# Performance work log

Hardware: AMD Instinct MI355X
Metric: run time of the kernel (lower is better)

The kernel has to match this reference:

```python
import jax, jax.numpy as jnp
from jax import lax
import numpy as np

# dims
V, D, T = 30000, 300, 24          # vocab, glove dim, seq len
H = 256                            # tweet_out_size == z_dim
NT, NU = 6000, 4000                # tweet nodes, user nodes
N = NT + NU
F, Z = 512, 256                    # user_feat_size, z_dim
E = 80000
B = 2000                           # batch_size (source tweets)
H1, H2, HEADS = 64, 100, 8
NEG = 0.2                          # GATConv default negative_slope


def setup_inputs() -> dict:
    k = jax.random.split(jax.random.key(0), 32)
    r = lambda i, shape, s=0.05: (s * jax.random.normal(k[i], shape)).astype(jnp.float32)
    return {
        "user_text": jax.random.randint(k[0], (B, T), 0, V),
        "user_feats": jax.random.normal(k[1], (NU, F), jnp.float32),
        "graph_node_features": jax.random.randint(k[2], (NT, T), 0, V),
        "graph_edge_index": jax.random.randint(k[3], (2, E), 0, N),
        "tweet_emb": r(4, (V, D), 0.1),
        "w_ih0": r(5, (3 * H, D)), "w_hh0": r(6, (3 * H, H)),
        "b_ih0": r(7, (3 * H,)), "b_hh0": r(8, (3 * H,)),
        "w_ih1": r(9, (3 * H, H)), "w_hh1": r(10, (3 * H, H)),
        "b_ih1": r(11, (3 * H,)), "b_hh1": r(12, (3 * H,)),
        "h0": r(13, (2, NT, H), 1.0),
        "w_mu": r(14, (Z, F)), "b_mu": r(15, (Z,)),
        "w_lv": r(16, (Z, F)), "b_lv": r(17, (Z,)),
        "w_dec": r(18, (F, Z)), "b_dec": r(19, (F,)),
        "vae_eps": r(20, (NU, Z), 1.0),
        "w1": r(21, (H, HEADS * H1)), "a_src1": r(22, (HEADS, H1)),
        "a_dst1": r(23, (HEADS, H1)), "b1": r(24, (HEADS * H1,)),
        "w2": r(25, (HEADS * H1, H2)), "a_src2": r(26, (1, H2)),
        "a_dst2": r(27, (1, H2)), "b2": r(28, (H2,)),
    }


def _gru_layer(x_seq, h0, w_ih, w_hh, b_ih, b_hh):
    # x_seq: [T, B, in]; torch nn.GRU gate math
    def step(h, x):
        gi = x @ w_ih.T + b_ih
        gh = h @ w_hh.T + b_hh
        i_r, i_z, i_n = jnp.split(gi, 3, axis=-1)
        h_r, h_z, h_n = jnp.split(gh, 3, axis=-1)
        r = jax.nn.sigmoid(i_r + h_r)
        z = jax.nn.sigmoid(i_z + h_z)
        n = jnp.tanh(i_n + r * h_n)
        hn = (1.0 - z) * n + z * h
        return hn, hn
    h_last, out = lax.scan(step, h0, x_seq)
    return out, h_last


def _gat(x, src, dst, w, a_src, a_dst, bias, heads, out_ch, concat):
    # PyG GATConv (eval mode, self-loops already appended)
    n = x.shape[0]
    xp = (x @ w).reshape(n, heads, out_ch)          # [N, H, C]
    as_n = (xp * a_src).sum(-1)                     # [N, H]
    ad_n = (xp * a_dst).sum(-1)
    e = jax.nn.leaky_relu(as_n[src] + ad_n[dst], NEG)          # [E, H]
    emax = jax.ops.segment_max(e, dst, num_segments=n)         # edge-softmax over dst
    ee = jnp.exp(e - emax[dst])
    denom = jax.ops.segment_sum(ee, dst, num_segments=n)
    alpha = ee / denom[dst]
    out = jax.ops.segment_sum(xp[src] * alpha[:, :, None], dst, num_segments=n)
    out = out.reshape(n, heads * out_ch) if concat else out.mean(axis=1)
    return out + bias


def reference(user_text, user_feats, graph_node_features, graph_edge_index,
              tweet_emb, w_ih0, w_hh0, b_ih0, b_hh0, w_ih1, w_hh1, b_ih1, b_hh1,
              h0, w_mu, b_mu, w_lv, b_lv, w_dec, b_dec, vae_eps,
              w1, a_src1, a_dst1, b1, w2, a_src2, a_dst2, b2):
    # --- VAE user embedding ---
    mu = user_feats @ w_mu.T + b_mu
    logvar = user_feats @ w_lv.T + b_lv
    z = mu + jnp.exp(0.5 * logvar) * vae_eps        # reparameterized latent
    rec = z @ w_dec.T + b_dec
    kl_loss = (-0.5 * (1.0 + logvar - mu**2 - jnp.exp(logvar)).sum(-1)).mean()
    rec_loss = ((rec - user_feats) ** 2).mean()
    # --- tweet encoder: embedding lookup + 2-layer GRU ---
    xe = tweet_emb[graph_node_features].transpose(1, 0, 2)     # [T, NT, D]
    out0, _ = _gru_layer(xe, h0[0], w_ih0, w_hh0, b_ih0, b_hh0)
    _, hn = _gru_layer(out0, h0[1], w_ih1, w_hh1, b_ih1, b_hh1)  # [NT, H]
    # --- assemble node features: source tweets, users, other tweets ---
    x_in = jnp.concatenate([hn[:B], z, hn[B:]], axis=0)        # [N, H]
    loops = jnp.arange(x_in.shape[0])
    src = jnp.concatenate([graph_edge_index[0], loops])
    dst = jnp.concatenate([graph_edge_index[1], loops])
    x1 = _gat(x_in, src, dst, w1, a_src1, a_dst1, b1, HEADS, H1, True)
    x2 = _gat(x1, src, dst, w2, a_src2, a_dst2, b2, 1, H2, False)
    return x2, kl_loss, rec_loss
```

## Files before the change

### kernel.cpp

```cpp
#include <hip/hip_runtime.h>

#define V_ 30000
#define D_ 300
#define DP_ 320
#define T_ 24
#define H_ 256
#define NT_ 6000
#define NU_ 4000
#define N_ 10000
#define F_ 512
#define Z_ 256
#define E_ 80000
#define B_ 2000
#define H1_ 64
#define H2_ 100
#define HEADS_ 8
#define E2_ (E_ + N_)

typedef __bf16 bf16_t;
typedef bf16_t bf16x8 __attribute__((ext_vector_type(8)));
typedef float  f32x4  __attribute__((ext_vector_type(4)));

__device__ __forceinline__ void gll16(const bf16_t* g, bf16_t* l)
{
    __builtin_amdgcn_global_load_lds(
        (const __attribute__((address_space(1))) void*)g,
        (__attribute__((address_space(3))) void*)l, 16, 0, 0);
}

struct GCfg {
    const bf16_t* A; const bf16_t* B; const float* bias;
    float* Cf; bf16_t* Cb; int M, N, K, ldc;
    const int* gtok; int t0;
};

template<bool OUTBF>
__global__ __launch_bounds__(256) void mfma_gemm(GCfg g0, GCfg g1)
{
    const GCfg g = blockIdx.z ? g1 : g0;
    __shared__ __align__(16) bf16_t SMEM[16384];
    const int tid  = (int)threadIdx.x;
    const int wave = tid >> 6, lane = tid & 63;
    const int quad = lane >> 4, l16 = lane & 15;
    const int mq = (wave & 1) * 64, nq = (wave >> 1) * 64;

    int bx = (int)blockIdx.x, by = (int)blockIdx.y;
    {
        int gx = (int)gridDim.x, total = gx * (int)gridDim.y;
        if ((total & 7) == 0) {
            int L = by * gx + bx;
            int F = (L & 7) * (total >> 3) + (L >> 3);
            bx = F % gx;
            by = F / gx;
        }
    }
    const int mbase = by * 128, nbase = bx * 128;
    const int M = g.M, N = g.N, K = g.K, ldc = g.ldc;

    const bf16_t* agp[2];
    const bf16_t* bgp[2];
#pragma unroll
    for (int j = 0; j < 2; j++) {
        int i = wave * 128 + j * 64 + lane;
        int c = i >> 7, row = i & 127;
        int r = mbase + row; if (r >= M) r = M - 1;
        int src = g.gtok ? g.gtok[(r % NT_) * T_ + g.t0 + (r / NT_)] : r;
        agp[j] = g.A + (size_t)src * K + c * 8;
        int rb = nbase + row; if (rb >= N) rb = N - 1;
        bgp[j] = g.B + (size_t)rb * K + c * 8;
    }

    f32x4 acc[4][4];
#pragma unroll
    for (int mi = 0; mi < 4; mi++)
#pragma unroll
        for (int ni = 0; ni < 4; ni++) acc[mi][ni] = (f32x4){0.f, 0.f, 0.f, 0.f};

    auto stage = [&](int b, int k0) {
        bf16_t* ab = SMEM + b * 4096 + wave * 1024;
        bf16_t* bb = SMEM + 8192 + b * 4096 + wave * 1024;
        gll16(agp[0] + k0, ab);
        gll16(agp[1] + k0, ab + 512);
        gll16(bgp[0] + k0, bb);
        gll16(bgp[1] + k0, bb + 512);
    };

    const int niter = K >> 5;
    stage(0, 0);
    for (int ks = 0; ks < niter; ks++) {
        __syncthreads();
        if (ks + 1 < niter) stage((ks + 1) & 1, (ks + 1) * 32);
        const bf16_t* Ab = SMEM + (ks & 1) * 4096;
        const bf16_t* Bb = SMEM + 8192 + (ks & 1) * 4096;
        bf16x8 afr[4], bfr[4];
#pragma unroll
        for (int mi = 0; mi < 4; mi++)
            afr[mi] = *(const bf16x8*)(Ab + (size_t)(quad * 128 + mq + mi * 16 + l16) * 8);
#pragma unroll
        for (int ni = 0; ni < 4; ni++)
            bfr[ni] = *(const bf16x8*)(Bb + (size_t)(quad * 128 + nq + ni * 16 + l16) * 8);
#pragma unroll
        for (int mi = 0; mi < 4; mi++)
#pragma unroll
            for (int ni = 0; ni < 4; ni++)
                acc[mi][ni] = __builtin_amdgcn_mfma_f32_16x16x32_bf16(
                    afr[mi], bfr[ni], acc[mi][ni], 0, 0, 0);
    }

    if (OUTBF) {
        __syncthreads();
#pragma unroll
        for (int ni = 0; ni < 4; ni++) {
            int colc = nq + ni * 16 + l16;
            float bv = g.bias ? g.bias[nbase + colc] : 0.f;
            int cc = colc >> 3, off = colc & 7;
#pragma unroll
            for (int mi = 0; mi < 4; mi++)
#pragma unroll
                for (int r = 0; r < 4; r++) {
                    int row = mq + mi * 16 + quad * 4 + r;
                    int sw = (row ^ (row >> 3)) & 7;
                    SMEM[row * 128 + ((cc ^ sw) << 3) + off] =
                        (bf16_t)(acc[mi][ni][r] + bv);
                }
        }
        __syncthreads();
        {
            int row = tid >> 1, seg = tid & 1;
            int sw = (row ^ (row >> 3)) & 7;
            int growr = mbase + row;
            if (growr < M) {
#pragma unroll
                for (int q = 0; q < 8; q++) {
                    int cc = seg * 8 + q;
                    bf16x8 v = *(const bf16x8*)(SMEM + row * 128 + ((cc ^ sw) << 3));
                    *(bf16x8*)(g.Cb + (size_t)growr * ldc + nbase + cc * 8) = v;
                }
            }
        }
    } else {
#pragma unroll
        for (int ni = 0; ni < 4; ni++) {
            int col = nbase + nq + ni * 16 + l16;
            if (col >= N) continue;
            float bv = g.bias ? g.bias[col] : 0.f;
#pragma unroll
            for (int mi = 0; mi < 4; mi++)
#pragma unroll
                for (int r = 0; r < 4; r++) {
                    int row = mbase + mq + mi * 16 + quad * 4 + r;
                    if (row >= M) continue;
                    g.Cf[(size_t)row * ldc + col] = acc[mi][ni][r] + bv;
                }
        }
    }
}

struct MegaLay {
    const bf16_t* vocGi;
    const int*    gnf;
    const bf16_t* whh0;
    const bf16_t* wih1;
    const bf16_t* whh1;
    const float *bhh0, *bih1, *bhh1;
    const bf16_t* h0in;
    const bf16_t* h1in;
    bf16_t*       h1out;
};

__device__ __forceinline__ float rcp_(float x)
{
    float r;
    asm("v_rcp_f32 %0, %1" : "=v"(r) : "v"(x));
    return r;
}
__device__ __forceinline__ float sigm_(float x)
{
    return rcp_(1.f + __expf(-x));
}
__device__ __forceinline__ float tanh_(float x)
{
    x = fminf(fmaxf(x, -15.f), 15.f);
    float t = __expf(2.f * x);
    return 1.f - 2.f * rcp_(t + 1.f);
}

#define HSW(Hb, row, byte) ((char*)(Hb) + ((((row) * 512) + (byte)) ^ (((row) & 7) << 4)))

__global__ __launch_bounds__(512, 1) void gru_mega(MegaLay L)
{
    __shared__ __align__(16) bf16_t H0L[8192];
    __shared__ __align__(16) bf16_t H1L[8192];
    __shared__ int TOK[768];
    const int tid  = (int)threadIdx.x;
    const int wv   = tid >> 6, lane = tid & 63;
    const int quad = lane >> 4, l16 = lane & 15;
    const int row0 = (int)blockIdx.x * 32;

    for (int i = tid; i < 768; i += 512) {
        int gi = row0 * T_ + i; if (gi >= NT_ * T_) gi = NT_ * T_ - 1;
        TOK[i] = L.gnf[gi];
    }
#pragma unroll
    for (int i = 0; i < 2; i++) {
        int idx  = i * 512 + tid;
        int rowl = idx >> 5, seg = idx & 31;
        int grow = row0 + rowl; if (grow >= NT_) grow = NT_ - 1;
        *(bf16x8*)HSW(H0L, rowl, seg * 16) =
            *(const bf16x8*)(L.h0in + (size_t)grow * H_ + seg * 8);
        *(bf16x8*)HSW(H1L, rowl, seg * 16) =
            *(const bf16x8*)(L.h1in + (size_t)grow * H_ + seg * 8);
    }

    float bh0[3][2], brz1[2][2], bni1[2], bnh1[2];
#pragma unroll
    for (int jj = 0; jj < 2; jj++) {
        int col = wv * 32 + jj * 16 + l16;
        bh0[0][jj] = L.bhh0[col];
        bh0[1][jj] = L.bhh0[256 + col];
        bh0[2][jj] = L.bhh0[512 + col];
        brz1[0][jj] = L.bih1[col] + L.bhh1[col];
        brz1[1][jj] = L.bih1[256 + col] + L.bhh1[256 + col];
        bni1[jj]    = L.bih1[512 + col];
        bnh1[jj]    = L.bhh1[512 + col];
    }

    auto run_gemm = [&](auto&& loadA, const bf16_t* W,
                        f32x4 (&arz)[2][2][2], f32x4 (&an)[2][2]) {
#pragma unroll 2
        for (int ks = 0; ks < 8; ks++) {
            bf16x8 bfr[3][2];
#pragma unroll
            for (int g = 0; g < 3; g++)
#pragma unroll
                for (int jj = 0; jj < 2; jj++)
                    bfr[g][jj] = *(const bf16x8*)(W +
                        (((size_t)(g * 16 + wv * 2 + jj) * 8 + ks) << 9) + lane * 8);
            bf16x8 afr[2];
            loadA(afr, ks);
#pragma unroll
            for (int m = 0; m < 2; m++)
#pragma unroll
                for (int jj = 0; jj < 2; jj++) {
                    arz[m][0][jj] = __builtin_amdgcn_mfma_f32_16x16x32_bf16(
                        afr[m], bfr[0][jj], arz[m][0][jj], 0, 0, 0);
                    arz[m][1][jj] = __builtin_amdgcn_mfma_f32_16x16x32_bf16(
                        afr[m], bfr[1][jj], arz[m][1][jj], 0, 0, 0);
                    an[m][jj] = __builtin_amdgcn_mfma_f32_16x16x32_bf16(
                        afr[m], bfr[2][jj], an[m][jj], 0, 0, 0);
                }
        }
    };

    __syncthreads();

    for (int t = 0; t < T_; t++) {
        float gi[2][2][4][3];
#pragma unroll
        for (int m = 0; m < 2; m++)
#pragma unroll
            for (int r2 = 0; r2 < 4; r2++) {
                int rowl = m * 16 + quad * 4 + r2;
                const bf16_t* gp = L.vocGi +
                    (size_t)TOK[rowl * T_ + t] * (3 * H_);
#pragma unroll
                for (int jj = 0; jj < 2; jj++) {
                    int col = wv * 32 + jj * 16 + l16;
#pragma unroll
                    for (int g = 0; g < 3; g++)
                        gi[m][jj][r2][g] = (float)gp[g * 256 + col];
                }
            }

        f32x4 arz[2][2][2], an_i[2][2], an_h[2][2];
#pragma unroll
        for (int m = 0; m < 2; m++)
#pragma unroll
            for (int jj = 0; jj < 2; jj++) {
                arz[m][0][jj] = (f32x4){0.f, 0.f, 0.f, 0.f};
                arz[m][1][jj] = (f32x4){0.f, 0.f, 0.f, 0.f};
                an_h[m][jj]   = (f32x4){0.f, 0.f, 0.f, 0.f};
            }

        run_gemm([&](bf16x8* afr, int ks) {
#pragma unroll
            for (int m = 0; m < 2; m++)
                afr[m] = *(const bf16x8*)HSW(H0L, m * 16 + l16,
                                             ks * 64 + quad * 16);
        }, L.whh0, arz, an_h);
        __syncthreads();

#pragma unroll
        for (int m = 0; m < 2; m++)
#pragma unroll
            for (int jj = 0; jj < 2; jj++) {
                int col = wv * 32 + jj * 16 + l16;
#pragma unroll
                for (int r = 0; r < 4; r++) {
                    int rowl = m * 16 + quad * 4 + r;
                    float hold = (float)*(const bf16_t*)HSW(H0L, rowl, col * 2);
                    float rg = sigm_(gi[m][jj][r][0] + arz[m][0][jj][r] + bh0[0][jj]);
                    float zg = sigm_(gi[m][jj][r][1] + arz[m][1][jj][r] + bh0[1][jj]);
                    float ng = tanh_(gi[m][jj][r][2] +
                                     rg * (an_h[m][jj][r] + bh0[2][jj]));
                    *(bf16_t*)HSW(H0L, rowl, col * 2) =
                        (bf16_t)((1.f - zg) * ng + zg * hold);
                }
            }
        __syncthreads();

#pragma unroll
        for (int m = 0; m < 2; m++)
#pragma unroll
            for (int jj = 0; jj < 2; jj++) {
                arz[m][0][jj] = (f32x4){0.f, 0.f, 0.f, 0.f};
                arz[m][1][jj] = (f32x4){0.f, 0.f, 0.f, 0.f};
                an_i[m][jj]   = (f32x4){0.f, 0.f, 0.f, 0.f};
                an_h[m][jj]   = (f32x4){0.f, 0.f, 0.f, 0.f};
            }
        run_gemm([&](bf16x8* afr, int ks) {
#pragma unroll
            for (int m = 0; m < 2; m++)
                afr[m] = *(const bf16x8*)HSW(H0L, m * 16 + l16,
                                             ks * 64 + quad * 16);
        }, L.wih1, arz, an_i);
        run_gemm([&](bf16x8* afr, int ks) {
#pragma unroll
            for (int m = 0; m < 2; m++)
                afr[m] = *(const bf16x8*)HSW(H1L, m * 16 + l16,
                                             ks * 64 + quad * 16);
        }, L.whh1, arz, an_h);
        __syncthreads();

#pragma unroll
        for (int m = 0; m < 2; m++)
#pragma unroll
            for (int jj = 0; jj < 2; jj++) {
                int col = wv * 32 + jj * 16 + l16;
#pragma unroll
                for (int r = 0; r < 4; r++) {
                    int rowl = m * 16 + quad * 4 + r;
                    float hold = (float)*(const bf16_t*)HSW(H1L, rowl, col * 2);
                    float rg = sigm_(arz[m][0][jj][r] + brz1[0][jj]);
                    float zg = sigm_(arz[m][1][jj][r] + brz1[1][jj]);
                    float ng = tanh_(an_i[m][jj][r] + bni1[jj] +
                                     rg * (an_h[m][jj][r] + bnh1[jj]));
                    *(bf16_t*)HSW(H1L, rowl, col * 2) =
                        (bf16_t)((1.f - zg) * ng + zg * hold);
                }
            }
    }

    __syncthreads();
#pragma unroll
    for (int i = 0; i < 2; i++) {
        int idx  = i * 512 + tid;
        int rowl = idx >> 5, seg = idx & 31;
        int grow = row0 + rowl;
        if (grow < NT_) {
            bf16x8 v = *(const bf16x8*)HSW(H1L, rowl, seg * 16);
            *(bf16x8*)(L.h1out + (size_t)grow * H_ + seg * 8) = v;
        }
    }
}

struct SegD { const float* src; bf16_t* dst; int rows, cin, cout, transp; };
struct PrepArgs { SegD seg[11]; long long base[12]; int nseg; long long total; };

__global__ void prep_kern(PrepArgs pa)
{
    long long stride = (long long)gridDim.x * blockDim.x;
    for (long long i = (long long)blockIdx.x * blockDim.x + threadIdx.x;
         i < pa.total; i += stride) {
        int k = 0;
        while (k + 1 < pa.nseg && i >= pa.base[k + 1]) k++;
        long long local = i - pa.base[k];
        SegD sg = pa.seg[k];
        float v;
        if (sg.transp == 2) {
            int nks  = sg.cout >> 5;
            int o    = (int)local;
            int e    = o & 7;
            int lane = (o >> 3) & 63;
            int rest = o >> 9;
            int ks   = rest % nks;
            int gcb  = rest / nks;
            int r    = (gcb >> 4) * 256 + (gcb & 15) * 16 + (lane & 15);
            int kk   = ks * 32 + (lane >> 4) * 8 + e;
            v = (kk < sg.cin) ? sg.src[(size_t)r * sg.cin + kk] : 0.f;
        } else {
            int r = (int)(local / sg.cout);
            int c = (int)(local - (long long)r * sg.cout);
            if (sg.transp) v = sg.src[(size_t)c * sg.rows + r];
            else           v = (c < sg.cin) ? sg.src[(size_t)r * sg.cin + c] : 0.f;
        }
        sg.dst[local] = (bf16_t)v;
    }
}

__global__ void init_all(const float* __restrict__ h0in, bf16_t* __restrict__ h0b,
                         bf16_t* __restrict__ h1b,
                         int* __restrict__ deg, int* __restrict__ dcnt,
                         float* __restrict__ loss2, float* __restrict__ b_ml,
                         const float* __restrict__ b_mu, const float* __restrict__ b_lv)
{
    int i = blockIdx.x * blockDim.x + threadIdx.x;
    if (i < NT_ * H_) {
        h0b[i] = (bf16_t)h0in[i];
        h1b[i] = (bf16_t)h0in[NT_ * H_ + i];
    }
    if (i < N_) { deg[i] = 0; dcnt[i] = 0; }
    if (i < 2 * Z_) b_ml[i] = (i < Z_) ? b_mu[i] : b_lv[i - Z_];
    if (i < 2) loss2[i] = 0.f;
}

__device__ __forceinline__ void edge_sd(const int* __restrict__ ei, int e, int& s, int& d)
{
    if (e < E_) { s = ei[e]; d = ei[E_ + e]; }
    else        { s = d = e - E_; }
}

__global__ void csr_hist(const int* __restrict__ ei, int* __restrict__ deg)
{
    int e = blockIdx.x * blockDim.x + threadIdx.x;
    if (e >= E2_) return;
    int s, d; edge_sd(ei, e, s, d);
    atomicAdd(deg + d, 1);
}

__global__ void csr_scan(const int* __restrict__ deg, int* __restrict__ rowptr)
{
    __shared__ int buf[256];
    __shared__ int carry;
    int tid = (int)threadIdx.x;
    if (tid == 0) { carry = 0; rowptr[0] = 0; }
    __syncthreads();
    for (int c0 = 0; c0 < N_; c0 += 256) {
        int i = c0 + tid;
        buf[tid] = (i < N_) ? deg[i] : 0;
        __syncthreads();
        for (int off = 1; off < 256; off <<= 1) {
            int t = (tid >= off) ? buf[tid - off] : 0;
            __syncthreads();
            buf[tid] += t;
            __syncthreads();
        }
        if (i < N_) rowptr[i + 1] = carry + buf[tid];
        __syncthreads();
        if (tid == 255) carry += buf[255];
        __syncthreads();
    }
}

__global__ void csr_scatter(const int* __restrict__ ei, const int* __restrict__ rowptr,
                            int* __restrict__ dcnt, int* __restrict__ csrc)
{
    int e = blockIdx.x * blockDim.x + threadIdx.x;
    if (e >= E2_) return;
    int s, d; edge_sd(ei, e, s, d);
    int pos = rowptr[d] + atomicAdd(dcnt + d, 1);
    csrc[pos] = s;
}

__global__ __launch_bounds__(256) void vae_z_kl(
    const float* __restrict__ ml, const float* __restrict__ eps,
    bf16_t* __restrict__ z_out, float* __restrict__ kl_out)
{
    float t = 0.f;
    int stride = (int)gridDim.x * 256;
    for (int idx = blockIdx.x * 256 + threadIdx.x; idx < NU_ * Z_; idx += stride) {
        int row = idx >> 8, c = idx & 255;
        float m = ml[(size_t)row * 512 + c];
        float l = ml[(size_t)row * 512 + 256 + c];
        float el = expf(l);
        z_out[idx] = (bf16_t)(m + expf(0.5f * l) * eps[idx]);
        t += -0.5f * (1.f + l - m * m - el);
    }
    __shared__ float red[256];
    red[threadIdx.x] = t;
    __syncthreads();
    for (int s = 128; s > 0; s >>= 1) {
        if ((int)threadIdx.x < s) red[threadIdx.x] += red[threadIdx.x + s];
        __syncthreads();
    }
    if (threadIdx.x == 0) atomicAdd(kl_out, red[0] * (1.f / NU_));
}

__global__ __launch_bounds__(256) void rec_loss_kern(
    const float* __restrict__ rec, const float* __restrict__ uf,
    float* __restrict__ loss_out)
{
    float t = 0.f;
    int stride = (int)gridDim.x * 256;
    for (int idx = blockIdx.x * 256 + threadIdx.x; idx < NU_ * F_; idx += stride) {
        float d = rec[idx] - uf[idx];
        t += d * d;
    }
    __shared__ float red[256];
    red[threadIdx.x] = t;
    __syncthreads();
    for (int s = 128; s > 0; s >>= 1) {
        if ((int)threadIdx.x < s) red[threadIdx.x] += red[threadIdx.x + s];
        __syncthreads();
    }
    if (threadIdx.x == 0) atomicAdd(loss_out, red[0] * (1.f / (NU_ * F_)));
}

__global__ void assemble_xin(const bf16_t* __restrict__ h1, bf16_t* __restrict__ x_in)
{
    int idx = blockIdx.x * blockDim.x + threadIdx.x;
    if (idx >= NT_ * H_) return;
    int row = idx >> 8, col = idx & 255;
    int dst = (row < B_) ? row : (row + NU_);
    x_in[(size_t)dst * H_ + col] = h1[idx];
}

__global__ void gat_attn_coef_bf(const bf16_t* __restrict__ xp,
                                 const float* __restrict__ a_src,
                                 const float* __restrict__ a_dst,
                                 float* __restrict__ asn, float* __restrict__ adn,
                                 int heads, int C)
{
    int i = blockIdx.x * blockDim.x + threadIdx.x;
    if (i >= N_ * heads) return;
    int node = i / heads, h = i - node * heads;
    const bf16_t* x = xp + (size_t)(node * heads + h) * C;
    float s = 0.f, d = 0.f;
    for (int c8 = 0; c8 < C; c8 += 8) {
        bf16x8 v = *(const bf16x8*)(x + c8);
#pragma unroll
        for (int j = 0; j < 8; j++) {
            float vv = (float)v[j];
            s += vv * a_src[h * C + c8 + j];
            d += vv * a_dst[h * C + c8 + j];
        }
    }
    asn[i] = s;
    adn[i] = d;
}

__global__ void gat_attn_coef(const float* __restrict__ xp, const float* __restrict__ a_src,
                              const float* __restrict__ a_dst, float* __restrict__ asn,
                              float* __restrict__ adn, int heads, int C)
{
    int i = blockIdx.x * blockDim.x + threadIdx.x;
    if (i >= N_ * heads) return;
    int node = i / heads, h = i - node * heads;
    const float* x = xp + (size_t)(node * heads + h) * C;
    float s = 0.f, d = 0.f;
    for (int c = 0; c < C; c++) {
        float v = x[c];
        s += v * a_src[h * C + c];
        d += v * a_dst[h * C + c];
    }
    asn[i] = s;
    adn[i] = d;
}

__global__ __launch_bounds__(256) void gat_agg1(
    const int* __restrict__ rowptr, const int* __restrict__ csrc,
    const float* __restrict__ asn, const float* __restrict__ adn,
    const bf16_t* __restrict__ xp, const float* __restrict__ bias,
    bf16_t* __restrict__ x1out)
{
    int d = blockIdx.x;
    int tid = (int)threadIdx.x;
    int beg = rowptr[d], end = rowptr[d + 1];
    int h0 = tid >> 6, h1 = h0 + 4;
    float ad0 = adn[d * 8 + h0], ad1 = adn[d * 8 + h1];
    float mx0 = -1e30f, mx1 = -1e30f;
    for (int e = beg; e < end; e++) {
        int s = csrc[e];
        float l0 = asn[s * 8 + h0] + ad0; l0 = (l0 > 0.f) ? l0 : 0.2f * l0;
        float l1 = asn[s * 8 + h1] + ad1; l1 = (l1 > 0.f) ? l1 : 0.2f * l1;
        mx0 = fmaxf(mx0, l0); mx1 = fmaxf(mx1, l1);
    }
    float den0 = 0.f, den1 = 0.f, acc0 = 0.f, acc1 = 0.f;
    for (int e = beg; e < end; e++) {
        int s = csrc[e];
        float l0 = asn[s * 8 + h0] + ad0; l0 = (l0 > 0.f) ? l0 : 0.2f * l0;
        float l1 = asn[s * 8 + h1] + ad1; l1 = (l1 > 0.f) ? l1 : 0.2f * l1;
        float p0 = expf(l0 - mx0), p1 = expf(l1 - mx1);
        den0 += p0; den1 += p1;
        acc0 += p0 * (float)xp[(size_t)s * 512 + tid];
        acc1 += p1 * (float)xp[(size_t)s * 512 + 256 + tid];
    }
    x1out[(size_t)d * 512 + tid]       = (bf16_t)(bias[tid] + acc0 / den0);
    x1out[(size_t)d * 512 + 256 + tid] = (bf16_t)(bias[256 + tid] + acc1 / den1);
}

__global__ __launch_bounds__(256) void gat_agg2(
    const int* __restrict__ rowptr, const int* __restrict__ csrc,
    const float* __restrict__ asn, const float* __restrict__ adn,
    const float* __restrict__ xp, const float* __restrict__ bias,
    float* __restrict__ outp)
{
    int d = blockIdx.x * 4 + ((int)threadIdx.x >> 6);
    if (d >= N_) return;
    int lane = (int)threadIdx.x & 63;
    int beg = rowptr[d], end = rowptr[d + 1];
    float adnd = adn[d];
    float mx = -1e30f;
    for (int e = beg; e < end; e++) {
        float l = asn[csrc[e]] + adnd;
        l = (l > 0.f) ? l : 0.2f * l;
        mx = fmaxf(mx, l);
    }
    float den = 0.f, acc0 = 0.f, acc1 = 0.f;
    for (int e = beg; e < end; e++) {
        int s = csrc[e];
        float l = asn[s] + adnd;
        l = (l > 0.f) ? l : 0.2f * l;
        float p = expf(l - mx);
        den += p;
        acc0 += p * xp[(size_t)s * H2_ + lane];
        if (lane < H2_ - 64) acc1 += p * xp[(size_t)s * H2_ + 64 + lane];
    }
    outp[(size_t)d * H2_ + lane] = bias[lane] + acc0 / den;
    if (lane < H2_ - 64)
        outp[(size_t)d * H2_ + 64 + lane] = bias[64 + lane] + acc1 / den;
}

extern "C" void kernel_launch(void* const* d_in, const int* in_sizes, int n_in,
                              void* d_out, int out_size, void* d_ws, size_t ws_size,
                              hipStream_t stream)
{
    const float* user_feats = (const float*)d_in[1];
    const int*   gnf        = (const int*)d_in[2];
    const int*   ei         = (const int*)d_in[3];
    const float* temb       = (const float*)d_in[4];
    const float* w_ih0      = (const float*)d_in[5];
    const float* w_hh0      = (const float*)d_in[6];
    const float* b_ih0      = (const float*)d_in[7];
    const float* b_hh0      = (const float*)d_in[8];
    const float* w_ih1      = (const float*)d_in[9];
    const float* w_hh1      = (const float*)d_in[10];
    const float* b_ih1      = (const float*)d_in[11];
    const float* b_hh1      = (const float*)d_in[12];
    const float* h0in       = (const float*)d_in[13];
    const float* w_mu       = (const float*)d_in[14];
    const float* b_mu       = (const float*)d_in[15];
    const float* w_lv       = (const float*)d_in[16];
    const float* b_lv       = (const float*)d_in[17];
    const float* w_dec      = (const float*)d_in[18];
    const float* b_dec      = (const float*)d_in[19];
    const float* veps       = (const float*)d_in[20];
    const float* w1         = (const float*)d_in[21];
    const float* a_src1     = (const float*)d_in[22];
    const float* a_dst1     = (const float*)d_in[23];
    const float* b1         = (const float*)d_in[24];
    const float* w2         = (const float*)d_in[25];
    const float* a_src2     = (const float*)d_in[26];
    const float* a_dst2     = (const float*)d_in[27];
    const float* b2         = (const float*)d_in[28];
    float* out = (float*)d_out;

    char* wsb = (char*)d_ws;
    bf16_t* temb_bf = (bf16_t*)(wsb + 0);
    bf16_t* vocGi   = (bf16_t*)(wsb + 19200000);
    float*  mlbuf   = (float*)(wsb + 66000000);
    float*  recb    = (float*)(wsb + 75000000);
    bf16_t* xp1b    = (bf16_t*)(wsb + 0);
    bf16_t* x1b     = (bf16_t*)(wsb + 20480000);
    float*  xp2     = (float*)(wsb + 30720000);
    bf16_t* wih0_bf = (bf16_t*)(wsb + 92928000);
    bf16_t* whh0_bf = (bf16_t*)(wsb + 93419520);
    bf16_t* wih1_bf = (bf16_t*)(wsb + 93812736);
    bf16_t* whh1_bf = (bf16_t*)(wsb + 94205952);
    bf16_t* wml_bf  = (bf16_t*)(wsb + 94599168);
    bf16_t* wdec_bf = (bf16_t*)(wsb + 95123456);
    bf16_t* w1t_bf  = (bf16_t*)(wsb + 95385600);
    bf16_t* w2t_bf  = (bf16_t*)(wsb + 95648000);
    float*  b_ml    = (float*)(wsb + 95750400);
    bf16_t* ufeats_bf = (bf16_t*)(wsb + 95752448);
    bf16_t* h0b_init = (bf16_t*)(wsb + 124424448);
    bf16_t* h1init  = (bf16_t*)(wsb + 127496448);
    bf16_t* h1sA    = (bf16_t*)(wsb + 130568448);
    bf16_t* xin_bf  = (bf16_t*)(wsb + 136712448);
    int*    deg     = (int*)(wsb + 141832448);
    int*    dcnt    = (int*)(wsb + 141872448);
    int*    rowptr  = (int*)(wsb + 141912448);
    int*    csrc    = (int*)(wsb + 141952512);
    float*  asn1    = (float*)(wsb + 142312512);
    float*  adn1    = (float*)(wsb + 142632512);
    float*  asn2    = (float*)(wsb + 142952512);
    float*  adn2    = (float*)(wsb + 142992512);

    const int TB = 256;
    auto blocks = [](int n) { return (n + 255) / 256; };

    auto mkcfg = [](const bf16_t* A, const bf16_t* B, const float* bias,
                    float* Cf, bf16_t* Cb, int M, int N, int K, int ldc,
                    const int* gtok, int t0) {
        GCfg g; g.A = A; g.B = B; g.bias = bias; g.Cf = Cf; g.Cb = Cb;
        g.M = M; g.N = N; g.K = K; g.ldc = ldc; g.gtok = gtok; g.t0 = t0;
        return g;
    };
    auto launch_bf = [&](GCfg g0) {
        dim3 grid((g0.N + 127) / 128, (g0.M + 127) / 128, 1);
        hipLaunchKernelGGL((mfma_gemm<true>), grid, dim3(TB), 0, stream, g0, g0);
    };
    auto launch_f32 = [&](GCfg g0) {
        dim3 grid((g0.N + 127) / 128, (g0.M + 127) / 128, 1);
        hipLaunchKernelGGL((mfma_gemm<false>), grid, dim3(TB), 0, stream, g0, g0);
    };

    PrepArgs pa;
    auto seg = [&](int k, const float* s, bf16_t* dst, int rows, int cin, int cout, int tr) {
        pa.seg[k] = SegD{s, dst, rows, cin, cout, tr};
    };
    seg(0, temb, temb_bf, V_, D_, DP_, 0);
    seg(1, w_ih0, wih0_bf, 3 * H_, D_, DP_, 0);
    seg(2, w_hh0, whh0_bf, 3 * H_, H_, H_, 2);
    seg(3, w_ih1, wih1_bf, 3 * H_, H_, H_, 2);
    seg(4, w_hh1, whh1_bf, 3 * H_, H_, H_, 2);
    seg(5, w_mu, wml_bf, Z_, F_, F_, 0);
    seg(6, w_lv, wml_bf + (size_t)Z_ * F_, Z_, F_, F_, 0);
    seg(7, w_dec, wdec_bf, F_, Z_, Z_, 0);
    seg(8, user_feats, ufeats_bf, NU_, F_, F_, 0);
    seg(9, w1, w1t_bf, HEADS_ * H1_, 0, H_, 1);
    seg(10, w2, w2t_bf, H2_, 0, HEADS_ * H1_, 1);
    pa.nseg = 11;
    long long acc = 0;
    for (int k = 0; k < 11; k++) {
        pa.base[k] = acc;
        acc += (long long)pa.seg[k].rows * pa.seg[k].cout;
    }
    pa.base[11] = acc;
    pa.total = acc;
    hipLaunchKernelGGL(prep_kern, dim3(6144), dim3(TB), 0, stream, pa);

    hipLaunchKernelGGL(init_all, dim3(blocks(NT_ * H_)), dim3(TB), 0, stream,
                       h0in, h0b_init, h1init,
                       deg, dcnt, out + N_ * H2_, b_ml, b_mu, b_lv);

    hipLaunchKernelGGL(csr_hist, dim3(blocks(E2_)), dim3(TB), 0, stream, ei, deg);
    hipLaunchKernelGGL(csr_scan, dim3(1), dim3(TB), 0, stream, deg, rowptr);
    hipLaunchKernelGGL(csr_scatter, dim3(blocks(E2_)), dim3(TB), 0, stream,
                       ei, rowptr, dcnt, csrc);

    launch_bf(mkcfg(temb_bf, wih0_bf, b_ih0, nullptr, vocGi,
                    V_, 3 * H_, DP_, 3 * H_, nullptr, 0));

    launch_f32(mkcfg(ufeats_bf, wml_bf, b_ml, mlbuf, nullptr,
                     NU_, 2 * Z_, F_, 2 * Z_, nullptr, 0));
    bf16_t* z_bf = xin_bf + (size_t)B_ * H_;
    hipLaunchKernelGGL(vae_z_kl, dim3(256), dim3(TB), 0, stream,
                       mlbuf, veps, z_bf, out + N_ * H2_);
    launch_f32(mkcfg(z_bf, wdec_bf, b_dec, recb, nullptr,
                     NU_, F_, Z_, F_, nullptr, 0));
    hipLaunchKernelGGL(rec_loss_kern, dim3(256), dim3(TB), 0, stream,
                       recb, user_feats, out + N_ * H2_ + 1);

    {
        MegaLay ML;
        ML.vocGi = vocGi; ML.gnf = gnf;
        ML.whh0 = whh0_bf; ML.wih1 = wih1_bf; ML.whh1 = whh1_bf;
        ML.bhh0 = b_hh0; ML.bih1 = b_ih1; ML.bhh1 = b_hh1;
        ML.h0in = h0b_init; ML.h1in = h1init; ML.h1out = h1sA;
        hipLaunchKernelGGL(gru_mega, dim3((NT_ + 31) / 32), dim3(512), 0, stream, ML);
    }

    hipLaunchKernelGGL(assemble_xin, dim3(blocks(NT_ * H_)), dim3(TB), 0, stream,
                       h1sA, xin_bf);

    launch_bf(mkcfg(xin_bf, w1t_bf, nullptr, nullptr, xp1b,
                    N_, HEADS_ * H1_, H_, HEADS_ * H1_, nullptr, 0));
    hipLaunchKernelGGL(gat_attn_coef_bf, dim3(blocks(N_ * HEADS_)), dim3(TB), 0, stream,
                       xp1b, a_src1, a_dst1, asn1, adn1, HEADS_, H1_);
    hipLaunchKernelGGL(gat_agg1, dim3(N_), dim3(TB), 0, stream,
                       rowptr, csrc, asn1, adn1, xp1b, b1, x1b);

    launch_f32(mkcfg(x1b, w2t_bf, nullptr, xp2, nullptr,
                     N_, H2_, HEADS_ * H1_, H2_, nullptr, 0));
    hipLaunchKernelGGL(gat_attn_coef, dim3(blocks(N_)), dim3(TB), 0, stream,
                       xp2, a_src2, a_dst2, asn2, adn2, 1, H2_);
    hipLaunchKernelGGL(gat_agg2, dim3((N_ + 3) / 4), dim3(TB), 0, stream,
                       rowptr, csrc, asn2, adn2, xp2, b2, out);

    (void)in_sizes; (void)n_in; (void)out_size; (void)ws_size;
}
```

Before: 835.8 us.

## Fuse GAT attention coefficients into aggregation with online softmax; scatter GRU output directly

The separate attention-coefficient kernels are removed. Each aggregation kernel now computes the source and destination scores per edge with wave-wide shuffle reductions, and uses a single-pass online softmax in place of the two-pass max-then-sum. The GRU kernel writes its final hidden state straight into the permuted x_in layout, which drops the assemble_xin kernel. The GRU input-gate values now seed the accumulators directly. This saves launches and one edge pass, but it recomputes per-source dot products for every edge and adds shuffle reductions and extra exps in the inner loop.

```diff
diff --git a/kernel.cpp b/kernel.cpp
--- a/kernel.cpp
+++ b/kernel.cpp
@@ -165,7 +165,7 @@
     const float *bhh0, *bih1, *bhh1;
     const bf16_t* h0in;
     const bf16_t* h1in;
-    bf16_t*       h1out;
+    bf16_t*       xinout;
 };
 
 __device__ __forceinline__ float rcp_(float x)
@@ -255,7 +255,8 @@
     __syncthreads();
 
     for (int t = 0; t < T_; t++) {
-        float gi[2][2][4][3];
+        f32x4 arz[2][2][2], an_i[2][2], an_h[2][2], gin[2][2];
+
 #pragma unroll
         for (int m = 0; m < 2; m++)
 #pragma unroll
@@ -266,21 +267,16 @@
 #pragma unroll
                 for (int jj = 0; jj < 2; jj++) {
                     int col = wv * 32 + jj * 16 + l16;
-#pragma unroll
-                    for (int g = 0; g < 3; g++)
-                        gi[m][jj][r2][g] = (float)gp[g * 256 + col];
+                    arz[m][0][jj][r2] = (float)gp[col];
+                    arz[m][1][jj][r2] = (float)gp[256 + col];
+                    gin[m][jj][r2]    = (float)gp[512 + col];
                 }
             }
-
-        f32x4 arz[2][2][2], an_i[2][2], an_h[2][2];
 #pragma unroll
         for (int m = 0; m < 2; m++)
 #pragma unroll
-            for (int jj = 0; jj < 2; jj++) {
-                arz[m][0][jj] = (f32x4){0.f, 0.f, 0.f, 0.f};
-                arz[m][1][jj] = (f32x4){0.f, 0.f, 0.f, 0.f};
-                an_h[m][jj]   = (f32x4){0.f, 0.f, 0.f, 0.f};
-            }
+            for (int jj = 0; jj < 2; jj++)
+                an_h[m][jj] = (f32x4){0.f, 0.f, 0.f, 0.f};
 
         run_gemm([&](bf16x8* afr, int ks) {
 #pragma unroll
@@ -299,9 +295,9 @@
                 for (int r = 0; r < 4; r++) {
                     int rowl = m * 16 + quad * 4 + r;
                     float hold = (float)*(const bf16_t*)HSW(H0L, rowl, col * 2);
-                    float rg = sigm_(gi[m][jj][r][0] + arz[m][0][jj][r] + bh0[0][jj]);
-                    float zg = sigm_(gi[m][jj][r][1] + arz[m][1][jj][r] + bh0[1][jj]);
-                    float ng = tanh_(gi[m][jj][r][2] +
+                    float rg = sigm_(arz[m][0][jj][r] + bh0[0][jj]);
+                    float zg = sigm_(arz[m][1][jj][r] + bh0[1][jj]);
+                    float ng = tanh_(gin[m][jj][r] +
                                      rg * (an_h[m][jj][r] + bh0[2][jj]));
                     *(bf16_t*)HSW(H0L, rowl, col * 2) =
                         (bf16_t)((1.f - zg) * ng + zg * hold);
@@ -358,8 +354,9 @@
         int rowl = idx >> 5, seg = idx & 31;
         int grow = row0 + rowl;
         if (grow < NT_) {
+            int dst = (grow < B_) ? grow : (grow + NU_);
             bf16x8 v = *(const bf16x8*)HSW(H1L, rowl, seg * 16);
-            *(bf16x8*)(L.h1out + (size_t)grow * H_ + seg * 8) = v;
+            *(bf16x8*)(L.xinout + (size_t)dst * H_ + seg * 8) = v;
         }
     }
 }
@@ -506,84 +503,47 @@
     if (threadIdx.x == 0) atomicAdd(loss_out, red[0] * (1.f / (NU_ * F_)));
 }
 
-__global__ void assemble_xin(const bf16_t* __restrict__ h1, bf16_t* __restrict__ x_in)
-{
-    int idx = blockIdx.x * blockDim.x + threadIdx.x;
-    if (idx >= NT_ * H_) return;
-    int row = idx >> 8, col = idx & 255;
-    int dst = (row < B_) ? row : (row + NU_);
-    x_in[(size_t)dst * H_ + col] = h1[idx];
-}
-
-__global__ void gat_attn_coef_bf(const bf16_t* __restrict__ xp,
-                                 const float* __restrict__ a_src,
-                                 const float* __restrict__ a_dst,
-                                 float* __restrict__ asn, float* __restrict__ adn,
-                                 int heads, int C)
-{
-    int i = blockIdx.x * blockDim.x + threadIdx.x;
-    if (i >= N_ * heads) return;
-    int node = i / heads, h = i - node * heads;
-    const bf16_t* x = xp + (size_t)(node * heads + h) * C;
-    float s = 0.f, d = 0.f;
-    for (int c8 = 0; c8 < C; c8 += 8) {
-        bf16x8 v = *(const bf16x8*)(x + c8);
-#pragma unroll
-        for (int j = 0; j < 8; j++) {
-            float vv = (float)v[j];
-            s += vv * a_src[h * C + c8 + j];
-            d += vv * a_dst[h * C + c8 + j];
-        }
-    }
-    asn[i] = s;
-    adn[i] = d;
-}
-
-__global__ void gat_attn_coef(const float* __restrict__ xp, const float* __restrict__ a_src,
-                              const float* __restrict__ a_dst, float* __restrict__ asn,
-                              float* __restrict__ adn, int heads, int C)
-{
-    int i = blockIdx.x * blockDim.x + threadIdx.x;
-    if (i >= N_ * heads) return;
-    int node = i / heads, h = i - node * heads;
-    const float* x = xp + (size_t)(node * heads + h) * C;
-    float s = 0.f, d = 0.f;
-    for (int c = 0; c < C; c++) {
-        float v = x[c];
-        s += v * a_src[h * C + c];
-        d += v * a_dst[h * C + c];
-    }
-    asn[i] = s;
-    adn[i] = d;
-}
-
 __global__ __launch_bounds__(256) void gat_agg1(
     const int* __restrict__ rowptr, const int* __restrict__ csrc,
-    const float* __restrict__ asn, const float* __restrict__ adn,
-    const bf16_t* __restrict__ xp, const float* __restrict__ bias,
+    const bf16_t* __restrict__ xp, const float* __restrict__ a_src,
+    const float* __restrict__ a_dst, const float* __restrict__ bias,
     bf16_t* __restrict__ x1out)
 {
     int d = blockIdx.x;
     int tid = (int)threadIdx.x;
+    int w = tid >> 6, lane = tid & 63;
+    int h0 = w, h1 = w + 4;
+    float as0 = a_src[h0 * 64 + lane], as1 = a_src[h1 * 64 + lane];
+    float adv0 = a_dst[h0 * 64 + lane], adv1 = a_dst[h1 * 64 + lane];
     int beg = rowptr[d], end = rowptr[d + 1];
-    int h0 = tid >> 6, h1 = h0 + 4;
-    float ad0 = adn[d * 8 + h0], ad1 = adn[d * 8 + h1];
-    float mx0 = -1e30f, mx1 = -1e30f;
-    for (int e = beg; e < end; e++) {
-        int s = csrc[e];
-        float l0 = asn[s * 8 + h0] + ad0; l0 = (l0 > 0.f) ? l0 : 0.2f * l0;
-        float l1 = asn[s * 8 + h1] + ad1; l1 = (l1 > 0.f) ? l1 : 0.2f * l1;
-        mx0 = fmaxf(mx0, l0); mx1 = fmaxf(mx1, l1);
-    }
+
+    float t0 = (float)xp[(size_t)d * 512 + tid] * adv0;
+    float t1 = (float)xp[(size_t)d * 512 + 256 + tid] * adv1;
+#pragma unroll
+    for (int mk = 1; mk < 64; mk <<= 1) {
+        t0 += __shfl_xor(t0, mk);
+        t1 += __shfl_xor(t1, mk);
+    }
+    float ad0 = t0, ad1 = t1;
+
+    float m0 = -1e30f, m1 = -1e30f;
     float den0 = 0.f, den1 = 0.f, acc0 = 0.f, acc1 = 0.f;
     for (int e = beg; e < end; e++) {
         int s = csrc[e];
-        float l0 = asn[s * 8 + h0] + ad0; l0 = (l0 > 0.f) ? l0 : 0.2f * l0;
-        float l1 = asn[s * 8 + h1] + ad1; l1 = (l1 > 0.f) ? l1 : 0.2f * l1;
-        float p0 = expf(l0 - mx0), p1 = expf(l1 - mx1);
-        den0 += p0; den1 += p1;
-        acc0 += p0 * (float)xp[(size_t)s * 512 + tid];
-        acc1 += p1 * (float)xp[(size_t)s * 512 + 256 + tid];
+        float x0 = (float)xp[(size_t)s * 512 + tid];
+        float x1 = (float)xp[(size_t)s * 512 + 256 + tid];
+        float s0 = x0 * as0, s1 = x1 * as1;
+#pragma unroll
+        for (int mk = 1; mk < 64; mk <<= 1) {
+            s0 += __shfl_xor(s0, mk);
+            s1 += __shfl_xor(s1, mk);
+        }
+        float l0 = s0 + ad0; l0 = (l0 > 0.f) ? l0 : 0.2f * l0;
+        float l1 = s1 + ad1; l1 = (l1 > 0.f) ? l1 : 0.2f * l1;
+        float M0 = fmaxf(m0, l0), sc0 = __expf(m0 - M0), p0 = __expf(l0 - M0);
+        den0 = den0 * sc0 + p0; acc0 = acc0 * sc0 + p0 * x0; m0 = M0;
+        float M1 = fmaxf(m1, l1), sc1 = __expf(m1 - M1), p1 = __expf(l1 - M1);
+        den1 = den1 * sc1 + p1; acc1 = acc1 * sc1 + p1 * x1; m1 = M1;
     }
     x1out[(size_t)d * 512 + tid]       = (bf16_t)(bias[tid] + acc0 / den0);
     x1out[(size_t)d * 512 + 256 + tid] = (bf16_t)(bias[256 + tid] + acc1 / den1);
@@ -591,33 +551,43 @@
 
 __global__ __launch_bounds__(256) void gat_agg2(
     const int* __restrict__ rowptr, const int* __restrict__ csrc,
-    const float* __restrict__ asn, const float* __restrict__ adn,
-    const float* __restrict__ xp, const float* __restrict__ bias,
+    const float* __restrict__ xp, const float* __restrict__ a_src,
+    const float* __restrict__ a_dst, const float* __restrict__ bias,
     float* __restrict__ outp)
 {
     int d = blockIdx.x * 4 + ((int)threadIdx.x >> 6);
     if (d >= N_) return;
     int lane = (int)threadIdx.x & 63;
+    int hi = (lane < H2_ - 64);
+    float a0 = a_src[lane], a1 = hi ? a_src[64 + lane] : 0.f;
+    float b0 = a_dst[lane], b1 = hi ? a_dst[64 + lane] : 0.f;
     int beg = rowptr[d], end = rowptr[d + 1];
-    float adnd = adn[d];
-    float mx = -1e30f;
-    for (int e = beg; e < end; e++) {
-        float l = asn[csrc[e]] + adnd;
-        l = (l > 0.f) ? l : 0.2f * l;
-        mx = fmaxf(mx, l);
-    }
-    float den = 0.f, acc0 = 0.f, acc1 = 0.f;
+
+    float xd0 = xp[(size_t)d * H2_ + lane];
+    float xd1 = hi ? xp[(size_t)d * H2_ + 64 + lane] : 0.f;
+    float t = xd0 * b0 + xd1 * b1;
+#pragma unroll
+    for (int mk = 1; mk < 64; mk <<= 1) t += __shfl_xor(t, mk);
+    float adnd = t;
+
+    float mx = -1e30f, den = 0.f, acc0 = 0.f, acc1 = 0.f;
     for (int e = beg; e < end; e++) {
         int s = csrc[e];
-        float l = asn[s] + adnd;
+        float x0 = xp[(size_t)s * H2_ + lane];
+        float x1 = hi ? xp[(size_t)s * H2_ + 64 + lane] : 0.f;
+        float sd = x0 * a0 + x1 * a1;
+#pragma unroll
+        for (int mk = 1; mk < 64; mk <<= 1) sd += __shfl_xor(sd, mk);
+        float l = sd + adnd;
         l = (l > 0.f) ? l : 0.2f * l;
-        float p = expf(l - mx);
-        den += p;
-        acc0 += p * xp[(size_t)s * H2_ + lane];
-        if (lane < H2_ - 64) acc1 += p * xp[(size_t)s * H2_ + 64 + lane];
+        float M = fmaxf(mx, l), sc = __expf(mx - M), p = __expf(l - M);
+        den = den * sc + p;
+        acc0 = acc0 * sc + p * x0;
+        acc1 = acc1 * sc + p * x1;
+        mx = M;
     }
     outp[(size_t)d * H2_ + lane] = bias[lane] + acc0 / den;
-    if (lane < H2_ - 64)
+    if (hi)
         outp[(size_t)d * H2_ + 64 + lane] = bias[64 + lane] + acc1 / den;
 }
 
@@ -675,16 +645,11 @@
     bf16_t* ufeats_bf = (bf16_t*)(wsb + 95752448);
     bf16_t* h0b_init = (bf16_t*)(wsb + 124424448);
     bf16_t* h1init  = (bf16_t*)(wsb + 127496448);
-    bf16_t* h1sA    = (bf16_t*)(wsb + 130568448);
     bf16_t* xin_bf  = (bf16_t*)(wsb + 136712448);
     int*    deg     = (int*)(wsb + 141832448);
     int*    dcnt    = (int*)(wsb + 141872448);
     int*    rowptr  = (int*)(wsb + 141912448);
     int*    csrc    = (int*)(wsb + 141952512);
-    float*  asn1    = (float*)(wsb + 142312512);
-    float*  adn1    = (float*)(wsb + 142632512);
-    float*  asn2    = (float*)(wsb + 142952512);
-    float*  adn2    = (float*)(wsb + 142992512);
 
     const int TB = 256;
     auto blocks = [](int n) { return (n + 255) / 256; };
@@ -757,26 +722,19 @@
         ML.vocGi = vocGi; ML.gnf = gnf;
         ML.whh0 = whh0_bf; ML.wih1 = wih1_bf; ML.whh1 = whh1_bf;
         ML.bhh0 = b_hh0; ML.bih1 = b_ih1; ML.bhh1 = b_hh1;
-        ML.h0in = h0b_init; ML.h1in = h1init; ML.h1out = h1sA;
+        ML.h0in = h0b_init; ML.h1in = h1init; ML.xinout = xin_bf;
         hipLaunchKernelGGL(gru_mega, dim3((NT_ + 31) / 32), dim3(512), 0, stream, ML);
     }
-
-    hipLaunchKernelGGL(assemble_xin, dim3(blocks(NT_ * H_)), dim3(TB), 0, stream,
-                       h1sA, xin_bf);
 
     launch_bf(mkcfg(xin_bf, w1t_bf, nullptr, nullptr, xp1b,
                     N_, HEADS_ * H1_, H_, HEADS_ * H1_, nullptr, 0));
-    hipLaunchKernelGGL(gat_attn_coef_bf, dim3(blocks(N_ * HEADS_)), dim3(TB), 0, stream,
-                       xp1b, a_src1, a_dst1, asn1, adn1, HEADS_, H1_);
     hipLaunchKernelGGL(gat_agg1, dim3(N_), dim3(TB), 0, stream,
-                       rowptr, csrc, asn1, adn1, xp1b, b1, x1b);
+                       rowptr, csrc, xp1b, a_src1, a_dst1, b1, x1b);
 
     launch_f32(mkcfg(x1b, w2t_bf, nullptr, xp2, nullptr,
                      N_, H2_, HEADS_ * H1_, H2_, nullptr, 0));
-    hipLaunchKernelGGL(gat_attn_coef, dim3(blocks(N_)), dim3(TB), 0, stream,
-                       xp2, a_src2, a_dst2, asn2, adn2, 1, H2_);
     hipLaunchKernelGGL(gat_agg2, dim3((N_ + 3) / 4), dim3(TB), 0, stream,
-                       rowptr, csrc, asn2, adn2, xp2, b2, out);
+                       rowptr, csrc, xp2, a_src2, a_dst2, b2, out);
 
     (void)in_sizes; (void)n_in; (void)out_size; (void)ws_size;
 }
```

Measured after the change: 794.2 us. -5.0%, faster.
